# Optimization experiments

Hardware: AMD Instinct MI355X
Metric: run time of the kernel (lower is better)

## Reference

```python
import jax, jax.numpy as jnp
import numpy as np

D_MODEL = 2048
D_INNER = 4096   # expand * d_model == ngroups * d_state
D_XB = 1024
N_HEADS = 32     # = ngroups
HEAD_DIM = 128   # = d_state
N_KV_HEADS = D_XB // HEAD_DIM  # 8
N_REP = N_HEADS // N_KV_HEADS  # 4
D_IN_PROJ = D_INNER + 2 * D_XB + D_INNER + N_HEADS  # 10272
ROPE_BASE = 10000.0


def setup_inputs() -> dict:
    key = jax.random.key(0)
    k1, k2, k3 = jax.random.split(key, 3)
    u = jax.random.normal(k1, (2, 2048, D_MODEL), dtype=jnp.float32)
    W_in = jax.random.normal(k2, (D_IN_PROJ, D_MODEL), dtype=jnp.float32) * (1.0 / np.sqrt(D_MODEL))
    W_out = jax.random.normal(k3, (D_MODEL, D_INNER), dtype=jnp.float32) * (1.0 / np.sqrt(D_INNER))
    return {"u": u, "W_in": W_in, "W_out": W_out}


def _rotate_half(x):
    x1, x2 = jnp.split(x, 2, axis=-1)
    return jnp.concatenate((-x2, x1), axis=-1)


def _rope_cos_sin(seqlen, dim, dtype):
    inv_freq = 1.0 / (ROPE_BASE ** (jnp.arange(0, dim, 2, dtype=jnp.float32) / dim))
    pos = jnp.arange(seqlen, dtype=jnp.float32)
    freqs = pos[:, None] * inv_freq[None, :]          # [S, dim/2]
    emb = jnp.concatenate((freqs, freqs), axis=-1)    # [S, dim]
    return jnp.cos(emb).astype(dtype), jnp.sin(emb).astype(dtype)


def reference(u, W_in, W_out):
    # NOTE: the module's forward short-circuits (early return) into a GQA
    # attention path; the SSM code after the return is dead.
    B, S, _ = u.shape
    zxbcdt = jnp.einsum('bsd,ed->bse', u, W_in)       # [B, S, D_IN_PROJ]
    # split: z (d_inner), x (d_xb), B (d_xb), C (d_inner), dt (nheads); d_mlp = 0
    o0 = D_INNER
    x = zxbcdt[..., o0:o0 + D_XB]
    Bm = zxbcdt[..., o0 + D_XB:o0 + 2 * D_XB]
    C = zxbcdt[..., o0 + 2 * D_XB:o0 + 2 * D_XB + D_INNER]
    # q = C (32 heads), k = B (8 heads), v = x (8 heads); [B, H, S, Dh]
    q = C.reshape(B, S, N_HEADS, HEAD_DIM).transpose(0, 2, 1, 3)
    k = Bm.reshape(B, S, N_KV_HEADS, HEAD_DIM).transpose(0, 2, 1, 3)
    v = x.reshape(B, S, N_KV_HEADS, HEAD_DIM).transpose(0, 2, 1, 3)
    cos, sin = _rope_cos_sin(S, HEAD_DIM, u.dtype)    # [S, Dh]
    cos = cos[None, None]                             # [1, 1, S, Dh]
    sin = sin[None, None]
    q = q * cos + _rotate_half(q) * sin
    k = k * cos + _rotate_half(k) * sin
    # repeat_kv: repeat_interleave along head dim
    k = jnp.repeat(k, N_REP, axis=1)
    v = jnp.repeat(v, N_REP, axis=1)
    scale = 1.0 / np.sqrt(HEAD_DIM)
    scores = jnp.einsum('bhqd,bhkd->bhqk', q, k) * scale
    causal = jnp.tril(jnp.ones((S, S), dtype=bool))
    scores = jnp.where(causal[None, None], scores, jnp.finfo(scores.dtype).min)
    attn = jax.nn.softmax(scores, axis=-1)
    out = jnp.einsum('bhqk,bhkd->bhqd', attn, v)      # [B, H, S, Dh]
    out = out.transpose(0, 2, 1, 3).reshape(B, S, D_INNER)
    return jnp.einsum('bse,de->bsd', out, W_out)      # [B, S, d_model]
```

## Files before the change

kernel.cpp:

```cpp
#include <hip/hip_runtime.h>
#include <stdint.h>

#define S_LEN 2048
#define BATCH 2
#define NH 32
#define NKV 8
#define HD 128
#define NE 6144

typedef __attribute__((ext_vector_type(8))) short short8;
typedef __attribute__((ext_vector_type(4))) float floatx4;

__device__ __forceinline__ unsigned short f2bf(float f) {
    union { float f; uint32_t u; } v; v.f = f;
    uint32_t u = v.u;
    u += 0x7FFFu + ((u >> 16) & 1u);
    return (unsigned short)(u >> 16);
}
__device__ __forceinline__ float bf2f(unsigned short h) {
    union { uint32_t u; float f; } v; v.u = ((uint32_t)h) << 16;
    return v.f;
}
__device__ __forceinline__ uint32_t cvt_pk_bf16(float lo, float hi) {
    uint32_t r;
    asm("v_cvt_pk_bf16_f32 %0, %1, %2" : "=v"(r) : "v"(lo), "v"(hi));
    return r;
}

__global__ void cast_f32_bf16(const float* __restrict__ in,
                              unsigned short* __restrict__ out, int n4) {
    int i = blockIdx.x * blockDim.x + threadIdx.x;
    if (i >= n4) return;
    float4 f = reinterpret_cast<const float4*>(in)[i];
    ushort4 o;
    o.x = f2bf(f.x); o.y = f2bf(f.y); o.z = f2bf(f.z); o.w = f2bf(f.w);
    reinterpret_cast<ushort4*>(out)[i] = o;
}

template <int OUT_BF16>
__global__ void __launch_bounds__(256)
gemm_bt(const unsigned short* __restrict__ A, const unsigned short* __restrict__ Bt,
        void* __restrict__ Cv, int M, int N, int K) {
    __shared__ unsigned short As[128 * 32];
    __shared__ unsigned short Bs[128 * 32];
    const int tid  = threadIdx.x;
    const int w    = tid >> 6;
    const int lane = tid & 63;
    const int quad = lane >> 4;
    const int l16  = lane & 15;
    const int wm   = w >> 1, wn = w & 1;
    const int m0 = blockIdx.y * 128, n0 = blockIdx.x * 128;

    floatx4 acc[4][4];
#pragma unroll
    for (int i = 0; i < 4; i++)
#pragma unroll
        for (int j = 0; j < 4; j++) acc[i][j] = {0.f, 0.f, 0.f, 0.f};

    const int lr = lane >> 2;
    const int lk = (lane & 3) * 8;
    const int KT = K >> 5;

    for (int kt = 0; kt < KT; ++kt) {
        const int k0 = kt << 5;
        __syncthreads();
#pragma unroll
        for (int c = 0; c < 2; ++c) {
            const int chunk = w * 2 + c;
            const unsigned short* ga = A  + (size_t)(m0 + chunk * 16 + lr) * K + k0 + lk;
            __builtin_amdgcn_global_load_lds(
                (const __attribute__((address_space(1))) void*)ga,
                (__attribute__((address_space(3))) void*)(As + chunk * 512), 16, 0, 0);
            const unsigned short* gb = Bt + (size_t)(n0 + chunk * 16 + lr) * K + k0 + lk;
            __builtin_amdgcn_global_load_lds(
                (const __attribute__((address_space(1))) void*)gb,
                (__attribute__((address_space(3))) void*)(Bs + chunk * 512), 16, 0, 0);
        }
        __syncthreads();
        short8 af[4], bf[4];
#pragma unroll
        for (int t = 0; t < 4; ++t) {
            af[t] = *reinterpret_cast<const short8*>(As + (wm * 64 + t * 16 + l16) * 32 + quad * 8);
            bf[t] = *reinterpret_cast<const short8*>(Bs + (wn * 64 + t * 16 + l16) * 32 + quad * 8);
        }
#pragma unroll
        for (int i = 0; i < 4; i++)
#pragma unroll
            for (int j = 0; j < 4; j++)
                acc[i][j] = __builtin_amdgcn_mfma_f32_16x16x32_bf16(af[i], bf[j], acc[i][j], 0, 0, 0);
    }

#pragma unroll
    for (int i = 0; i < 4; i++)
#pragma unroll
        for (int j = 0; j < 4; j++) {
            const int row = m0 + wm * 64 + i * 16 + quad * 4;
            const int col = n0 + wn * 64 + j * 16 + l16;
#pragma unroll
            for (int r = 0; r < 4; r++) {
                float vv = acc[i][j][r];
                if (OUT_BF16)
                    ((unsigned short*)Cv)[(size_t)(row + r) * N + col] = f2bf(vv);
                else
                    ((float*)Cv)[(size_t)(row + r) * N + col] = vv;
            }
        }
}

#define QSCALE 0.12748539509360f
__global__ void rope_split(const unsigned short* __restrict__ Z,
                           unsigned short* __restrict__ Q,
                           unsigned short* __restrict__ Kb,
                           unsigned short* __restrict__ Vt) {
    const int PER_TOK = 2048 + 512 + 1024;
    int idx = blockIdx.x * blockDim.x + threadIdx.x;
    if (idx >= BATCH * S_LEN * PER_TOK) return;
    int t = idx / PER_TOK;
    int r = idx - t * PER_TOK;
    int b = t / S_LEN, s = t - b * S_LEN;
    const unsigned short* z = Z + (size_t)t * NE;
    if (r < 2048) {
        int h = r >> 6, j = r & 63;
        float x0 = bf2f(z[2048 + h * 128 + j]);
        float x1 = bf2f(z[2048 + h * 128 + j + 64]);
        float inv = exp2f((float)j * -0.20762050593f);
        float c, sn; sincosf((float)s * inv, &sn, &c);
        size_t base = ((size_t)(b * NH + h) * S_LEN + s) * HD;
        Q[base + j]      = f2bf((x0 * c - x1 * sn) * QSCALE);
        Q[base + j + 64] = f2bf((x1 * c + x0 * sn) * QSCALE);
    } else if (r < 2560) {
        int rr = r - 2048; int kh = rr >> 6, j = rr & 63;
        float x0 = bf2f(z[1024 + kh * 128 + j]);
        float x1 = bf2f(z[1024 + kh * 128 + j + 64]);
        float inv = exp2f((float)j * -0.20762050593f);
        float c, sn; sincosf((float)s * inv, &sn, &c);
        size_t base = ((size_t)(b * NKV + kh) * S_LEN + s) * HD;
        Kb[base + j]      = f2bf(x0 * c - x1 * sn);
        Kb[base + j + 64] = f2bf(x1 * c + x0 * sn);
    } else {
        int m = r - 2560; int kh = m >> 7, d = m & 127;
        int k = s & 63;
        int kp = (k & 32) + ((k & 15) << 1) + ((k >> 4) & 1);
        int sp = (s & ~63) | kp;
        Vt[((size_t)(b * NKV + kh) * HD + d) * S_LEN + sp] = z[m];
    }
}

template <bool DIAG>
__device__ __forceinline__ void attn_tile(
    const short8 (&qf)[4], floatx4 (&oacc)[8], float (&lsum)[4],
    const unsigned short* __restrict__ Ks, const unsigned short* __restrict__ Vs,
    unsigned short* __restrict__ pw, int w, int quad, int l16) {
    const int e = l16 & 7;

    floatx4 sacc[4];
#pragma unroll
    for (int nb = 0; nb < 4; nb++) sacc[nb] = {0.f, 0.f, 0.f, 0.f};
    __builtin_amdgcn_s_setprio(1);
#pragma unroll
    for (int ks = 0; ks < 4; ++ks) {
#pragma unroll
        for (int nb = 0; nb < 4; ++nb) {
            const int srow = nb * 16 + l16;
            const int pc = (ks * 4 + quad) ^ e;
            short8 kf = *reinterpret_cast<const short8*>(Ks + srow * 128 + pc * 8);
            sacc[nb] = __builtin_amdgcn_mfma_f32_16x16x32_bf16(qf[ks], kf, sacc[nb], 0, 0, 0);
        }
    }
    __builtin_amdgcn_s_setprio(0);

    float pv[4][4];
#pragma unroll
    for (int nb = 0; nb < 4; ++nb)
#pragma unroll
        for (int r = 0; r < 4; ++r) {
            float p = exp2f(sacc[nb][r]);
            if (DIAG)
                p = (nb * 16 + l16 <= w * 16 + quad * 4 + r) ? p : 0.0f;
            pv[nb][r] = p;
            lsum[r] += p;
        }

    const int row0 = quad * 4;
    const int sub = l16 >> 2, off = (l16 & 3) * 2;
#pragma unroll
    for (int r = 0; r < 4; ++r) {
        const int rowe = (row0 + r) & 7;
#pragma unroll
        for (int g = 0; g < 2; ++g) {
            uint32_t pk = cvt_pk_bf16(pv[g * 2][r], pv[g * 2 + 1][r]);
            const int chunk = (g * 4 + sub) ^ rowe;
            *reinterpret_cast<uint32_t*>(pw + (row0 + r) * 64 + chunk * 8 + off) = pk;
        }
    }

    __builtin_amdgcn_s_setprio(1);
#pragma unroll
    for (int kv_sub = 0; kv_sub < 2; ++kv_sub) {
        const int pcP = (kv_sub * 4 + quad) ^ e;
        short8 pf = *reinterpret_cast<const short8*>(pw + l16 * 64 + pcP * 8);
#pragma unroll
        for (int dt = 0; dt < 8; ++dt) {
            const int drow = dt * 16 + l16;
            const int pcV = (kv_sub * 4 + quad) ^ e;
            short8 vf = *reinterpret_cast<const short8*>(Vs + drow * 64 + pcV * 8);
            oacc[dt] = __builtin_amdgcn_mfma_f32_16x16x32_bf16(pf, vf, oacc[dt], 0, 0, 0);
        }
    }
    __builtin_amdgcn_s_setprio(0);
}

__global__ void __launch_bounds__(256, 4)
attn_kernel(const unsigned short* __restrict__ Q,
            const unsigned short* __restrict__ Kb,
            const unsigned short* __restrict__ Vt,
            unsigned short* __restrict__ Ob) {
    __shared__ unsigned short Ks[64 * 128];
    __shared__ unsigned short Vs[128 * 64];
    __shared__ unsigned short Ps[4][16 * 64];
    const int tid  = threadIdx.x;
    const int w    = tid >> 6;
    const int lane = tid & 63;
    const int quad = lane >> 4;
    const int l16  = lane & 15;
    const int blk = blockIdx.x;
    const int qt = 31 - (blk >> 6);
    const int bh = blk & 63;
    const int h = bh & 31, b = bh >> 5;
    const int kvh = h >> 2;
    const int qw0 = qt * 64 + w * 16;

    const unsigned short* Qbase = Q  + ((size_t)(b * NH  + h)   * S_LEN) * HD;
    const unsigned short* Kbase = Kb + ((size_t)(b * NKV + kvh) * S_LEN) * HD;
    const unsigned short* Vbase = Vt + ((size_t)(b * NKV + kvh) * HD) * S_LEN;

    short8 qf[4];
    {
        const unsigned short* qrow = Qbase + (size_t)(qw0 + l16) * HD + quad * 8;
#pragma unroll
        for (int ks = 0; ks < 4; ++ks)
            qf[ks] = *reinterpret_cast<const short8*>(qrow + ks * 32);
    }

    floatx4 oacc[8];
#pragma unroll
    for (int i = 0; i < 8; i++) oacc[i] = {0.f, 0.f, 0.f, 0.f};
    float lsum[4] = {0.f, 0.f, 0.f, 0.f};

    const unsigned short* kp[4];
    const unsigned short* vp[4];
#pragma unroll
    for (int c = 0; c < 4; ++c) {
        const int bI = w * 4 + c;
        const int krow = bI * 4 + (lane >> 4);
        kp[c] = Kbase + (size_t)krow * HD + ((lane & 15) ^ (krow & 7)) * 8;
        const int drow = bI * 8 + (lane >> 3);
        vp[c] = Vbase + (size_t)drow * S_LEN + ((lane & 7) ^ (drow & 7)) * 8;
    }

#define STAGE() do {                                                           \
    _Pragma("unroll")                                                          \
    for (int c = 0; c < 4; ++c) {                                              \
        const int bI = w * 4 + c;                                              \
        __builtin_amdgcn_global_load_lds(                                      \
            (const __attribute__((address_space(1))) void*)kp[c],              \
            (__attribute__((address_space(3))) void*)(Ks + bI * 512), 16, 0, 0);\
        __builtin_amdgcn_global_load_lds(                                      \
            (const __attribute__((address_space(1))) void*)vp[c],              \
            (__attribute__((address_space(3))) void*)(Vs + bI * 512), 16, 0, 0);\
        kp[c] += 64 * HD; vp[c] += 64;                                         \
    }                                                                          \
} while (0)

    unsigned short* pw = &Ps[w][0];

    for (int t = 0; t < qt; ++t) {
        __syncthreads();
        STAGE();
        __syncthreads();
        attn_tile<false>(qf, oacc, lsum, Ks, Vs, pw, w, quad, l16);
    }
    __syncthreads();
    STAGE();
    __syncthreads();
    attn_tile<true>(qf, oacc, lsum, Ks, Vs, pw, w, quad, l16);
#undef STAGE

    float linv[4];
#pragma unroll
    for (int r = 0; r < 4; ++r) {
        float s = lsum[r];
#pragma unroll
        for (int off = 1; off < 16; off <<= 1) s += __shfl_xor(s, off);
        linv[r] = 1.0f / s;
    }
#pragma unroll
    for (int dt = 0; dt < 8; ++dt) {
        const int d = dt * 16 + l16;
#pragma unroll
        for (int r = 0; r < 4; ++r) {
            const int row = qw0 + quad * 4 + r;
            Ob[((size_t)(b * S_LEN + row)) * 4096 + h * 128 + d] = f2bf(oacc[dt][r] * linv[r]);
        }
    }
}

extern "C" void kernel_launch(void* const* d_in, const int* in_sizes, int n_in,
                              void* d_out, int out_size, void* d_ws, size_t ws_size,
                              hipStream_t stream) {
    const float* u     = (const float*)d_in[0];
    const float* W_in  = (const float*)d_in[1];
    const float* W_out = (const float*)d_in[2];
    float* out = (float*)d_out;

    char* ws = (char*)d_ws;
    unsigned short* u_bf    = (unsigned short*)(ws);
    unsigned short* win_bf  = (unsigned short*)(ws + 16777216);
    unsigned short* wout_bf = (unsigned short*)(ws + 41943040);
    unsigned short* Z       = (unsigned short*)(ws + 58720256);
    unsigned short* Qb      = (unsigned short*)(ws + 109051904);
    unsigned short* Kv      = (unsigned short*)(ws + 142606336);
    unsigned short* Vt      = (unsigned short*)(ws + 150994944);
    unsigned short* Ob      = (unsigned short*)(ws + 159383552);

    {
        int n4 = (2 * 2048 * 2048) / 4;
        cast_f32_bf16<<<(n4 + 255) / 256, 256, 0, stream>>>(u, u_bf, n4);
        n4 = (6144 * 2048) / 4;
        cast_f32_bf16<<<(n4 + 255) / 256, 256, 0, stream>>>(W_in + (size_t)4096 * 2048, win_bf, n4);
        n4 = (2048 * 4096) / 4;
        cast_f32_bf16<<<(n4 + 255) / 256, 256, 0, stream>>>(W_out, wout_bf, n4);
    }
    {
        dim3 g(6144 / 128, 4096 / 128);
        gemm_bt<1><<<g, 256, 0, stream>>>(u_bf, win_bf, Z, 4096, 6144, 2048);
    }
    {
        int n = BATCH * S_LEN * 3584;
        rope_split<<<(n + 255) / 256, 256, 0, stream>>>(Z, Qb, Kv, Vt);
    }
    attn_kernel<<<BATCH * NH * (S_LEN / 64), 256, 0, stream>>>(Qb, Kv, Vt, Ob);
    {
        dim3 g(2048 / 128, 4096 / 128);
        gemm_bt<0><<<g, 256, 0, stream>>>(Ob, wout_bf, out, 2048 == 2048 ? 4096 : 4096, 2048, 4096);
    }
}
```

Before: 549.2 us.

## Add 256x256-tile pipelined GEMM with direct-to-LDS loads for input projection

Replaces the 128x128-tile GEMM used for the input projection with a new 512-thread kernel that computes 256x256 tiles. It stages tiles with global_load_lds into double-buffered, XOR-swizzled LDS, interleaves prefetch with MFMA phases under raised wave priority, and remaps block indices to improve L2 locality. Larger tiles raise arithmetic intensity and overlap loads with compute, at the cost of heavy register use (128 accumulator floats per thread) and a grid of only 384 blocks, which may leave CUs unevenly loaded.

```diff
diff --git a/kernel.cpp b/kernel.cpp
--- a/kernel.cpp
+++ b/kernel.cpp
@@ -104,6 +104,176 @@
                 else
                     ((float*)Cv)[(size_t)(row + r) * N + col] = vv;
             }
+        }
+}
+
+__device__ __forceinline__ short8 ldfrag256(const unsigned short* base, int row, int k8) {
+    const int c8 = k8 ^ ((row & 4) ? 2 : 0);
+    return *reinterpret_cast<const short8*>(base + row * 64 + c8 * 8);
+}
+
+__global__ void __launch_bounds__(512, 2)
+gemm256_bt(const unsigned short* __restrict__ A, const unsigned short* __restrict__ Bt,
+           unsigned short* __restrict__ C, int M, int N, int K) {
+    __shared__ unsigned short As[2][256 * 64];
+    __shared__ unsigned short Bs[2][256 * 64];
+    const int tid  = threadIdx.x;
+    const int w    = tid >> 6;
+    const int lane = tid & 63;
+    const int quad = lane >> 4;
+    const int l16  = lane & 15;
+    const int wm   = w >> 2, wn = w & 3;
+
+    const int nwg = gridDim.x * gridDim.y;
+    const int cpx = nwg >> 3;
+    const int lin = blockIdx.y * gridDim.x + blockIdx.x;
+    const int swz = (lin & 7) * cpx + (lin >> 3);
+    const int ntx = N >> 8;
+    const int m0 = (swz / ntx) << 8;
+    const int n0 = (swz % ntx) << 8;
+
+    floatx4 acc[8][4];
+#pragma unroll
+    for (int i = 0; i < 8; i++)
+#pragma unroll
+        for (int j = 0; j < 4; j++) acc[i][j] = {0.f, 0.f, 0.f, 0.f};
+
+    const int l8  = lane >> 3;
+    const int c8s = (lane & 7) ^ (((lane >> 5) & 1) << 1);
+    const unsigned short* apA = A  + (size_t)(m0 + w * 16 + l8) * K + c8s * 8;
+    const unsigned short* apB = Bt + (size_t)(n0 + w * 16 + l8) * K + c8s * 8;
+
+#define GLD256(src, dst) __builtin_amdgcn_global_load_lds(                     \
+    (const __attribute__((address_space(1))) void*)(src),                      \
+    (__attribute__((address_space(3))) void*)(dst), 16, 0, 0)
+
+#define STAGE_A256(bufi, t) do {                                               \
+    unsigned short* d = &As[bufi][w * 16 * 64];                                \
+    const unsigned short* s = apA + (size_t)(t) * 64;                          \
+    GLD256(s,                    d);                                           \
+    GLD256(s + (size_t)8 * K,    d + 8 * 64);                                  \
+    GLD256(s + (size_t)128 * K,  d + 128 * 64);                                \
+    GLD256(s + (size_t)136 * K,  d + 136 * 64);                                \
+} while (0)
+
+#define STAGE_B256(bufi, t) do {                                               \
+    unsigned short* d = &Bs[bufi][w * 16 * 64];                                \
+    const unsigned short* s = apB + (size_t)(t) * 64;                          \
+    GLD256(s,                    d);                                           \
+    GLD256(s + (size_t)8 * K,    d + 8 * 64);                                  \
+    GLD256(s + (size_t)128 * K,  d + 128 * 64);                                \
+    GLD256(s + (size_t)136 * K,  d + 136 * 64);                                \
+} while (0)
+
+    STAGE_A256(0, 0); STAGE_B256(0, 0);
+    STAGE_A256(1, 1); STAGE_B256(1, 1);
+
+    short8 a0[8], a1[8], b0[4], b1[4];
+    const int NT = K >> 6;
+
+#pragma unroll 1
+    for (int t = 0; t < NT; ++t) {
+        const int buf = t & 1;
+        const unsigned short* Ab = &As[buf][0];
+        const unsigned short* Bb = &Bs[buf][0];
+
+        if (t < NT - 1) { asm volatile("s_waitcnt vmcnt(8)" ::: "memory"); }
+        else            { asm volatile("s_waitcnt vmcnt(0)" ::: "memory"); }
+        __builtin_amdgcn_s_barrier();
+        asm volatile("" ::: "memory");
+
+#pragma unroll
+        for (int mi = 0; mi < 4; ++mi) {
+            const int row = wm * 128 + mi * 16 + l16;
+            a0[mi * 2 + 0] = ldfrag256(Ab, row, quad);
+            a0[mi * 2 + 1] = ldfrag256(Ab, row, 4 + quad);
+        }
+#pragma unroll
+        for (int ni = 0; ni < 2; ++ni) {
+            const int row = wn * 64 + ni * 16 + l16;
+            b0[ni * 2 + 0] = ldfrag256(Bb, row, quad);
+            b0[ni * 2 + 1] = ldfrag256(Bb, row, 4 + quad);
+        }
+        asm volatile("" ::: "memory");
+        __builtin_amdgcn_s_barrier();
+        __builtin_amdgcn_s_setprio(1);
+#pragma unroll
+        for (int mi = 0; mi < 4; ++mi)
+#pragma unroll
+            for (int ni = 0; ni < 2; ++ni) {
+                acc[mi][ni] = __builtin_amdgcn_mfma_f32_16x16x32_bf16(a0[mi*2+0], b0[ni*2+0], acc[mi][ni], 0, 0, 0);
+                acc[mi][ni] = __builtin_amdgcn_mfma_f32_16x16x32_bf16(a0[mi*2+1], b0[ni*2+1], acc[mi][ni], 0, 0, 0);
+            }
+        __builtin_amdgcn_s_setprio(0);
+        asm volatile("" ::: "memory");
+        __builtin_amdgcn_s_barrier();
+
+#pragma unroll
+        for (int mi = 0; mi < 4; ++mi) {
+            const int row = wm * 128 + 64 + mi * 16 + l16;
+            a1[mi * 2 + 0] = ldfrag256(Ab, row, quad);
+            a1[mi * 2 + 1] = ldfrag256(Ab, row, 4 + quad);
+        }
+#pragma unroll
+        for (int ni = 0; ni < 2; ++ni) {
+            const int row = wn * 64 + 32 + ni * 16 + l16;
+            b1[ni * 2 + 0] = ldfrag256(Bb, row, quad);
+            b1[ni * 2 + 1] = ldfrag256(Bb, row, 4 + quad);
+        }
+        asm volatile("" ::: "memory");
+        __builtin_amdgcn_s_barrier();
+        __builtin_amdgcn_s_setprio(1);
+#pragma unroll
+        for (int mi = 0; mi < 4; ++mi)
+#pragma unroll
+            for (int ni = 0; ni < 2; ++ni) {
+                acc[4 + mi][ni] = __builtin_amdgcn_mfma_f32_16x16x32_bf16(a1[mi*2+0], b0[ni*2+0], acc[4+mi][ni], 0, 0, 0);
+                acc[4 + mi][ni] = __builtin_amdgcn_mfma_f32_16x16x32_bf16(a1[mi*2+1], b0[ni*2+1], acc[4+mi][ni], 0, 0, 0);
+            }
+        __builtin_amdgcn_s_setprio(0);
+        asm volatile("" ::: "memory");
+        __builtin_amdgcn_s_barrier();
+
+        if (t + 2 < NT) { STAGE_A256(buf, t + 2); }
+        asm volatile("" ::: "memory");
+        __builtin_amdgcn_s_barrier();
+        __builtin_amdgcn_s_setprio(1);
+#pragma unroll
+        for (int mi = 0; mi < 4; ++mi)
+#pragma unroll
+            for (int ni = 0; ni < 2; ++ni) {
+                acc[4 + mi][2 + ni] = __builtin_amdgcn_mfma_f32_16x16x32_bf16(a1[mi*2+0], b1[ni*2+0], acc[4+mi][2+ni], 0, 0, 0);
+                acc[4 + mi][2 + ni] = __builtin_amdgcn_mfma_f32_16x16x32_bf16(a1[mi*2+1], b1[ni*2+1], acc[4+mi][2+ni], 0, 0, 0);
+            }
+        __builtin_amdgcn_s_setprio(0);
+        asm volatile("" ::: "memory");
+        __builtin_amdgcn_s_barrier();
+
+        if (t + 2 < NT) { STAGE_B256(buf, t + 2); }
+        asm volatile("" ::: "memory");
+        __builtin_amdgcn_s_setprio(1);
+#pragma unroll
+        for (int mi = 0; mi < 4; ++mi)
+#pragma unroll
+            for (int ni = 0; ni < 2; ++ni) {
+                acc[mi][2 + ni] = __builtin_amdgcn_mfma_f32_16x16x32_bf16(a0[mi*2+0], b1[ni*2+0], acc[mi][2+ni], 0, 0, 0);
+                acc[mi][2 + ni] = __builtin_amdgcn_mfma_f32_16x16x32_bf16(a0[mi*2+1], b1[ni*2+1], acc[mi][2+ni], 0, 0, 0);
+            }
+        __builtin_amdgcn_s_setprio(0);
+    }
+#undef STAGE_A256
+#undef STAGE_B256
+#undef GLD256
+
+#pragma unroll
+    for (int mi = 0; mi < 8; ++mi)
+#pragma unroll
+        for (int ni = 0; ni < 4; ++ni) {
+            const int row = m0 + wm * 128 + mi * 16 + quad * 4;
+            const int col = n0 + wn * 64 + ni * 16 + l16;
+#pragma unroll
+            for (int r = 0; r < 4; ++r)
+                C[(size_t)(row + r) * N + col] = f2bf(acc[mi][ni][r]);
         }
 }
 
@@ -332,8 +502,8 @@
         cast_f32_bf16<<<(n4 + 255) / 256, 256, 0, stream>>>(W_out, wout_bf, n4);
     }
     {
-        dim3 g(6144 / 128, 4096 / 128);
-        gemm_bt<1><<<g, 256, 0, stream>>>(u_bf, win_bf, Z, 4096, 6144, 2048);
+        dim3 g(6144 / 256, 4096 / 256);
+        gemm256_bt<<<g, 512, 0, stream>>>(u_bf, win_bf, Z, 4096, 6144, 2048);
     }
     {
         int n = BATCH * S_LEN * 3584;
@@ -342,6 +512,6 @@
     attn_kernel<<<BATCH * NH * (S_LEN / 64), 256, 0, stream>>>(Qb, Kv, Vt, Ob);
     {
         dim3 g(2048 / 128, 4096 / 128);
-        gemm_bt<0><<<g, 256, 0, stream>>>(Ob, wout_bf, out, 2048 == 2048 ? 4096 : 4096, 2048, 4096);
-    }
-}
+        gemm_bt<0><<<g, 256, 0, stream>>>(Ob, wout_bf, out, 4096, 2048, 4096);
+    }
+}
```

Measured after the change: 547.2 us. No clear change (-0.4%).

## Replace bf16 GEMM with 256x128 triple-buffered swizzled pipelined kernel

Applied to the files above, without the earlier changes.

Replaces the single-buffered 128x128 GEMM with a 512-thread kernel that computes 256x128 tiles over K-steps of 64. It triple-buffers LDS, loading through global_load_lds two stages ahead and waiting with vmcnt, so memory traffic overlaps the MFMA work. It adds an XOR swizzle on the LDS layout to avoid bank conflicts, remaps workgroups across blocks for cache locality, and raises wave priority around the MFMA bursts. The cost is a large LDS footprint (about 144KB), which limits occupancy to one block per CU, and more complex barrier choreography.

```diff
diff --git a/kernel.cpp b/kernel.cpp
--- a/kernel.cpp
+++ b/kernel.cpp
@@ -37,19 +37,31 @@
     reinterpret_cast<ushort4*>(out)[i] = o;
 }
 
+__device__ __forceinline__ short8 ldfragg(const unsigned short* base, int row, int k8) {
+    const int c8 = k8 ^ (row & 7);
+    return *reinterpret_cast<const short8*>(base + row * 64 + c8 * 8);
+}
+
 template <int OUT_BF16>
-__global__ void __launch_bounds__(256)
-gemm_bt(const unsigned short* __restrict__ A, const unsigned short* __restrict__ Bt,
-        void* __restrict__ Cv, int M, int N, int K) {
-    __shared__ unsigned short As[128 * 32];
-    __shared__ unsigned short Bs[128 * 32];
+__global__ void __launch_bounds__(512, 2)
+gemm_256x128(const unsigned short* __restrict__ A, const unsigned short* __restrict__ Bt,
+             void* __restrict__ Cv, int M, int N, int K) {
+    __shared__ unsigned short As[3][256 * 64];
+    __shared__ unsigned short Bs[3][128 * 64];
     const int tid  = threadIdx.x;
     const int w    = tid >> 6;
     const int lane = tid & 63;
     const int quad = lane >> 4;
     const int l16  = lane & 15;
     const int wm   = w >> 1, wn = w & 1;
-    const int m0 = blockIdx.y * 128, n0 = blockIdx.x * 128;
+
+    const int nwg = gridDim.x * gridDim.y;
+    const int cpx = nwg >> 3;
+    const int lin = blockIdx.y * gridDim.x + blockIdx.x;
+    const int swz = (lin & 7) * cpx + (lin >> 3);
+    const int ntx = N >> 7;
+    const int m0 = (swz / ntx) << 8;
+    const int n0 = (swz % ntx) << 7;
 
     floatx4 acc[4][4];
 #pragma unroll
@@ -57,48 +69,103 @@
 #pragma unroll
         for (int j = 0; j < 4; j++) acc[i][j] = {0.f, 0.f, 0.f, 0.f};
 
-    const int lr = lane >> 2;
-    const int lk = (lane & 3) * 8;
-    const int KT = K >> 5;
-
-    for (int kt = 0; kt < KT; ++kt) {
-        const int k0 = kt << 5;
-        __syncthreads();
-#pragma unroll
-        for (int c = 0; c < 2; ++c) {
-            const int chunk = w * 2 + c;
-            const unsigned short* ga = A  + (size_t)(m0 + chunk * 16 + lr) * K + k0 + lk;
-            __builtin_amdgcn_global_load_lds(
-                (const __attribute__((address_space(1))) void*)ga,
-                (__attribute__((address_space(3))) void*)(As + chunk * 512), 16, 0, 0);
-            const unsigned short* gb = Bt + (size_t)(n0 + chunk * 16 + lr) * K + k0 + lk;
-            __builtin_amdgcn_global_load_lds(
-                (const __attribute__((address_space(1))) void*)gb,
-                (__attribute__((address_space(3))) void*)(Bs + chunk * 512), 16, 0, 0);
-        }
-        __syncthreads();
-        short8 af[4], bf[4];
-#pragma unroll
-        for (int t = 0; t < 4; ++t) {
-            af[t] = *reinterpret_cast<const short8*>(As + (wm * 64 + t * 16 + l16) * 32 + quad * 8);
-            bf[t] = *reinterpret_cast<const short8*>(Bs + (wn * 64 + t * 16 + l16) * 32 + quad * 8);
-        }
-#pragma unroll
-        for (int i = 0; i < 4; i++)
-#pragma unroll
-            for (int j = 0; j < 4; j++)
-                acc[i][j] = __builtin_amdgcn_mfma_f32_16x16x32_bf16(af[i], bf[j], acc[i][j], 0, 0, 0);
-    }
-
-#pragma unroll
-    for (int i = 0; i < 4; i++)
-#pragma unroll
-        for (int j = 0; j < 4; j++) {
-            const int row = m0 + wm * 64 + i * 16 + quad * 4;
-            const int col = n0 + wn * 64 + j * 16 + l16;
-#pragma unroll
-            for (int r = 0; r < 4; r++) {
-                float vv = acc[i][j][r];
+    const int l8  = lane >> 3;
+    const int c8s = (lane & 7) ^ ((lane >> 3) & 7);
+    const unsigned short* apA = A  + (size_t)(m0 + w * 32 + l8) * K + c8s * 8;
+    const unsigned short* apB = Bt + (size_t)(n0 + w * 16 + l8) * K + c8s * 8;
+
+#define GLD(src, dst) __builtin_amdgcn_global_load_lds(                        \
+    (const __attribute__((address_space(1))) void*)(src),                      \
+    (__attribute__((address_space(3))) void*)(dst), 16, 0, 0)
+
+#define STG1(bufi, t) do {                     \
+    unsigned short* d = &As[bufi][w * 32 * 64];                                \
+    const unsigned short* s = apA + (size_t)(t) * 64;                          \
+    GLD(s,                   d);                                               \
+    GLD(s + (size_t)8  * K,  d + 8  * 64);                                     \
+    GLD(s + (size_t)16 * K,  d + 16 * 64);                                     \
+} while (0)
+
+#define STG2(bufi, t) do {              \
+    unsigned short* dA = &As[bufi][w * 32 * 64];                               \
+    const unsigned short* sA = apA + (size_t)(t) * 64;                         \
+    GLD(sA + (size_t)24 * K, dA + 24 * 64);                                    \
+    unsigned short* dB = &Bs[bufi][w * 16 * 64];                               \
+    const unsigned short* sB = apB + (size_t)(t) * 64;                         \
+    GLD(sB,                  dB);                                              \
+    GLD(sB + (size_t)8 * K,  dB + 8 * 64);                                     \
+} while (0)
+
+    STG1(0, 0); STG2(0, 0);
+    STG1(1, 1); STG2(1, 1);
+
+    const int NT = K >> 6;
+    int bufc = 0;
+
+#pragma unroll 1
+    for (int t = 0; t < NT; ++t) {
+        const unsigned short* Ab = &As[bufc][0];
+        const unsigned short* Bb = &Bs[bufc][0];
+        const int bufn = (bufc + 2 >= 3) ? bufc - 1 : bufc + 2;
+
+        if (t < NT - 1) { asm volatile("s_waitcnt vmcnt(6)" ::: "memory"); }
+        else            { asm volatile("s_waitcnt vmcnt(0)" ::: "memory"); }
+        __builtin_amdgcn_s_barrier();
+        asm volatile("" ::: "memory");
+
+        short8 a0[4], b0[4];
+#pragma unroll
+        for (int mi = 0; mi < 4; ++mi)
+            a0[mi] = ldfragg(Ab, wm * 64 + mi * 16 + l16, quad);
+#pragma unroll
+        for (int ni = 0; ni < 4; ++ni)
+            b0[ni] = ldfragg(Bb, wn * 64 + ni * 16 + l16, quad);
+        if (t + 2 < NT) { STG1(bufn, t + 2); }
+        asm volatile("" ::: "memory");
+        __builtin_amdgcn_s_barrier();
+        __builtin_amdgcn_s_setprio(1);
+#pragma unroll
+        for (int mi = 0; mi < 4; ++mi)
+#pragma unroll
+            for (int ni = 0; ni < 4; ++ni)
+                acc[mi][ni] = __builtin_amdgcn_mfma_f32_16x16x32_bf16(a0[mi], b0[ni], acc[mi][ni], 0, 0, 0);
+        __builtin_amdgcn_s_setprio(0);
+        asm volatile("" ::: "memory");
+        __builtin_amdgcn_s_barrier();
+
+        short8 a1[4], b1[4];
+#pragma unroll
+        for (int mi = 0; mi < 4; ++mi)
+            a1[mi] = ldfragg(Ab, wm * 64 + mi * 16 + l16, 4 + quad);
+#pragma unroll
+        for (int ni = 0; ni < 4; ++ni)
+            b1[ni] = ldfragg(Bb, wn * 64 + ni * 16 + l16, 4 + quad);
+        if (t + 2 < NT) { STG2(bufn, t + 2); }
+        asm volatile("" ::: "memory");
+        __builtin_amdgcn_s_barrier();
+        __builtin_amdgcn_s_setprio(1);
+#pragma unroll
+        for (int mi = 0; mi < 4; ++mi)
+#pragma unroll
+            for (int ni = 0; ni < 4; ++ni)
+                acc[mi][ni] = __builtin_amdgcn_mfma_f32_16x16x32_bf16(a1[mi], b1[ni], acc[mi][ni], 0, 0, 0);
+        __builtin_amdgcn_s_setprio(0);
+
+        bufc = (bufc + 1 >= 3) ? 0 : bufc + 1;
+    }
+#undef STG1
+#undef STG2
+#undef GLD
+
+#pragma unroll
+    for (int mi = 0; mi < 4; ++mi)
+#pragma unroll
+        for (int ni = 0; ni < 4; ++ni) {
+            const int row = m0 + wm * 64 + mi * 16 + quad * 4;
+            const int col = n0 + wn * 64 + ni * 16 + l16;
+#pragma unroll
+            for (int r = 0; r < 4; ++r) {
+                float vv = acc[mi][ni][r];
                 if (OUT_BF16)
                     ((unsigned short*)Cv)[(size_t)(row + r) * N + col] = f2bf(vv);
                 else
@@ -332,8 +399,8 @@
         cast_f32_bf16<<<(n4 + 255) / 256, 256, 0, stream>>>(W_out, wout_bf, n4);
     }
     {
-        dim3 g(6144 / 128, 4096 / 128);
-        gemm_bt<1><<<g, 256, 0, stream>>>(u_bf, win_bf, Z, 4096, 6144, 2048);
+        dim3 g(6144 / 128, 4096 / 256);
+        gemm_256x128<1><<<g, 512, 0, stream>>>(u_bf, win_bf, Z, 4096, 6144, 2048);
     }
     {
         int n = BATCH * S_LEN * 3584;
@@ -341,7 +408,7 @@
     }
     attn_kernel<<<BATCH * NH * (S_LEN / 64), 256, 0, stream>>>(Qb, Kv, Vt, Ob);
     {
-        dim3 g(2048 / 128, 4096 / 128);
-        gemm_bt<0><<<g, 256, 0, stream>>>(Ob, wout_bf, out, 2048 == 2048 ? 4096 : 4096, 2048, 4096);
-    }
-}
+        dim3 g(2048 / 128, 4096 / 256);
+        gemm_256x128<0><<<g, 512, 0, stream>>>(Ob, wout_bf, out, 4096, 2048, 4096);
+    }
+}
```

Result: faster. 494.2 us (-10.0%).
